# Performance work log

Measured on AMD Instinct MI355X. Metric: run time of the kernel, lower is better.

The kernel has to match this reference:

```python
import jax, jax.numpy as jnp
import numpy as np

B, H, S, DK = 2, 8, 4096, 64


def setup_inputs() -> dict:
    key = jax.random.key(0)
    kq, kk, kv = jax.random.split(key, 3)
    Q = jax.random.normal(kq, (B, H, S, DK), dtype=jnp.float32)
    K = jax.random.normal(kk, (B, H, S, DK), dtype=jnp.float32)
    V = jax.random.normal(kv, (B, H, S, DK), dtype=jnp.float32)
    attn_mask = jnp.zeros((1,), dtype=bool)  # accepted but unused by the module
    return {"Q": Q, "K": K, "V": V, "attn_mask": attn_mask}


def reference(Q, K, V, attn_mask):
    d_k = Q.shape[-1]
    scale = 1.0 / np.sqrt(d_k).astype(np.float32)
    # scores: [b, h, q, k] -- full O(n^2) matrix, as in the original
    scores = jnp.einsum('bhqd,bhkd->bhqk', Q, K) * scale
    attn = jax.nn.softmax(scores, axis=-1)
    context = jnp.einsum('bhqk,bhkd->bhqd', attn, V)
    return (context, attn)
```

## Files before the change

kernel.cpp:

```cpp
#include <hip/hip_runtime.h>
#include <hip/hip_bf16.h>


typedef __bf16 bf16x8 __attribute__((ext_vector_type(8)));
typedef __bf16 bf16x4 __attribute__((ext_vector_type(4)));
typedef float f32x4 __attribute__((ext_vector_type(4)));

#define BH 16
#define SEQ 4096
#define DKD 64

__global__ void cvt_bf16_kernel(const float* __restrict__ src,
                                __bf16* __restrict__ dst, int n4, float scale) {
    int i = blockIdx.x * blockDim.x + threadIdx.x;
    if (i < n4) {
        const float4 v = reinterpret_cast<const float4*>(src)[i];
        bf16x4 o;
        o[0] = (__bf16)(v.x * scale); o[1] = (__bf16)(v.y * scale);
        o[2] = (__bf16)(v.z * scale); o[3] = (__bf16)(v.w * scale);
        reinterpret_cast<bf16x4*>(dst)[i] = o;
    }
}

__global__ void transpose_v_kernel(const float* __restrict__ V,
                                   __bf16* __restrict__ Vt) {
    __shared__ __bf16 T[DKD][72];
    const int head = blockIdx.y;
    const int s0 = blockIdx.x * 64;
    const int t = threadIdx.x;
    const float* vp = V + ((size_t)head * SEQ + s0) * DKD;
#pragma unroll
    for (int i = 0; i < 16; ++i) {
        int j = i * 256 + t;
        T[j & 63][j >> 6] = (__bf16)vp[j];
    }
    __syncthreads();
    __bf16* op = Vt + (size_t)head * DKD * SEQ + s0;
#pragma unroll
    for (int i = 0; i < 16; ++i) {
        int j = i * 256 + t;
        op[(size_t)(j >> 6) * SEQ + (j & 63)] = T[j >> 6][j & 63];
    }
}

__global__ __launch_bounds__(128, 4) void attn_kernel(
    const __bf16* __restrict__ Qb, const __bf16* __restrict__ Kb,
    const __bf16* __restrict__ Vt, float* __restrict__ out_ctx,
    float* __restrict__ out_attn) {
    __shared__ __align__(16) float P32[2][16][68];

    const int tid = threadIdx.x;
    const int w = tid >> 6;
    const int lane = tid & 63;
    const int c16 = lane & 15;
    const int g = lane >> 4;
    const int head = blockIdx.y;
    const int qbase = blockIdx.x * 32 + w * 16;

    const __bf16* qp = Qb + ((size_t)head * SEQ + qbase + c16) * DKD + g * 8;
    const bf16x8 qf0 = *reinterpret_cast<const bf16x8*>(qp);
    const bf16x8 qf1 = *reinterpret_cast<const bf16x8*>(qp + 32);

    const __bf16* kbase = Kb + (size_t)head * SEQ * DKD;

    float lsum[4] = {0.f, 0.f, 0.f, 0.f};
    for (int kt = 0; kt < SEQ; kt += 64) {
        f32x4 acc[4];
#pragma unroll
        for (int ct = 0; ct < 4; ++ct) {
            acc[ct] = (f32x4){0.f, 0.f, 0.f, 0.f};
            const __bf16* kp = kbase + (size_t)(kt + ct * 16 + c16) * DKD + g * 8;
            bf16x8 kf0 = *reinterpret_cast<const bf16x8*>(kp);
            bf16x8 kf1 = *reinterpret_cast<const bf16x8*>(kp + 32);
            acc[ct] = __builtin_amdgcn_mfma_f32_16x16x32_bf16(qf0, kf0, acc[ct], 0, 0, 0);
            acc[ct] = __builtin_amdgcn_mfma_f32_16x16x32_bf16(qf1, kf1, acc[ct], 0, 0, 0);
        }
#pragma unroll
        for (int r = 0; r < 4; ++r) {
            lsum[r] += (__expf(acc[0][r]) + __expf(acc[1][r])) +
                       (__expf(acc[2][r]) + __expf(acc[3][r]));
        }
    }

    float inv_l[4];
#pragma unroll
    for (int r = 0; r < 4; ++r) {
        float t = lsum[r];
        t += __shfl_xor(t, 1);
        t += __shfl_xor(t, 2);
        t += __shfl_xor(t, 4);
        t += __shfl_xor(t, 8);
        inv_l[r] = 1.0f / t;
    }

    f32x4 o[4];
#pragma unroll
    for (int dt = 0; dt < 4; ++dt) o[dt] = (f32x4){0.f, 0.f, 0.f, 0.f};

    float* attn_p = out_attn + ((size_t)head * SEQ + qbase) * SEQ;
    const __bf16* vbase = Vt + (size_t)head * DKD * SEQ;

    for (int kt = 0; kt < SEQ; kt += 64) {
        f32x4 acc[4];
#pragma unroll
        for (int ct = 0; ct < 4; ++ct) {
            acc[ct] = (f32x4){0.f, 0.f, 0.f, 0.f};
            const __bf16* kp = kbase + (size_t)(kt + ct * 16 + c16) * DKD + g * 8;
            bf16x8 kf0 = *reinterpret_cast<const bf16x8*>(kp);
            bf16x8 kf1 = *reinterpret_cast<const bf16x8*>(kp + 32);
            acc[ct] = __builtin_amdgcn_mfma_f32_16x16x32_bf16(qf0, kf0, acc[ct], 0, 0, 0);
            acc[ct] = __builtin_amdgcn_mfma_f32_16x16x32_bf16(qf1, kf1, acc[ct], 0, 0, 0);
        }
#pragma unroll
        for (int ct = 0; ct < 4; ++ct) {
#pragma unroll
            for (int r = 0; r < 4; ++r) {
                P32[w][g * 4 + r][ct * 16 + c16] = __expf(acc[ct][r]) * inv_l[r];
            }
        }
        asm volatile("" ::: "memory");

#pragma unroll
        for (int r4 = 0; r4 < 4; ++r4) {
            const int row = r4 * 4 + g;
            f32x4 v = *reinterpret_cast<const f32x4*>(&P32[w][row][c16 * 4]);
            __builtin_nontemporal_store(
                v, reinterpret_cast<f32x4*>(attn_p + (size_t)row * SEQ + kt + c16 * 4));
        }

        f32x4 pr0 = *reinterpret_cast<const f32x4*>(&P32[w][c16][g * 8]);
        f32x4 pr1 = *reinterpret_cast<const f32x4*>(&P32[w][c16][g * 8 + 4]);
        f32x4 pr2 = *reinterpret_cast<const f32x4*>(&P32[w][c16][g * 8 + 32]);
        f32x4 pr3 = *reinterpret_cast<const f32x4*>(&P32[w][c16][g * 8 + 36]);
        bf16x8 pa0, pa1;
#pragma unroll
        for (int j = 0; j < 4; ++j) {
            pa0[j] = (__bf16)pr0[j];
            pa0[j + 4] = (__bf16)pr1[j];
            pa1[j] = (__bf16)pr2[j];
            pa1[j + 4] = (__bf16)pr3[j];
        }
#pragma unroll
        for (int dt = 0; dt < 4; ++dt) {
            const __bf16* vp2 = vbase + (size_t)(dt * 16 + c16) * SEQ + kt + g * 8;
            bf16x8 vf0 = *reinterpret_cast<const bf16x8*>(vp2);
            bf16x8 vf1 = *reinterpret_cast<const bf16x8*>(vp2 + 32);
            o[dt] = __builtin_amdgcn_mfma_f32_16x16x32_bf16(pa0, vf0, o[dt], 0, 0, 0);
            o[dt] = __builtin_amdgcn_mfma_f32_16x16x32_bf16(pa1, vf1, o[dt], 0, 0, 0);
        }
        asm volatile("" ::: "memory");
    }

    float* ctx_p = out_ctx + ((size_t)head * SEQ + qbase) * DKD;
#pragma unroll
    for (int dt = 0; dt < 4; ++dt)
#pragma unroll
        for (int r = 0; r < 4; ++r)
            ctx_p[(size_t)(g * 4 + r) * DKD + dt * 16 + c16] = o[dt][r];
}

extern "C" void kernel_launch(void* const* d_in, const int* in_sizes, int n_in,
                              void* d_out, int out_size, void* d_ws, size_t ws_size,
                              hipStream_t stream) {
    const float* Q = (const float*)d_in[0];
    const float* K = (const float*)d_in[1];
    const float* V = (const float*)d_in[2];
    float* out = (float*)d_out;

    const size_t nElem = (size_t)BH * SEQ * DKD;
    __bf16* Qb = (__bf16*)d_ws;
    __bf16* Kb = Qb + nElem;
    __bf16* Vt = Kb + nElem;

    float* out_ctx = out;
    float* out_attn = out + nElem;

    const int n4 = (int)(nElem / 4);
    cvt_bf16_kernel<<<dim3((n4 + 255) / 256), dim3(256), 0, stream>>>(Q, Qb, n4, 0.125f);
    cvt_bf16_kernel<<<dim3((n4 + 255) / 256), dim3(256), 0, stream>>>(K, Kb, n4, 1.0f);
    transpose_v_kernel<<<dim3(64, BH), dim3(256), 0, stream>>>(V, Vt);
    attn_kernel<<<dim3(SEQ / 32, BH), dim3(128), 0, stream>>>(Qb, Kb, Vt, out_ctx, out_attn);
}
```

Baseline: 726.1 us.

## Swap MFMA operand order, fold log2e into Q scale, software-pipeline S and PV

Swaps the MFMA operands so each lane holds a contiguous run of four scores for one query row. That lets the fp32 attention probabilities be stored straight from registers, drops the fp32 LDS staging, and cuts the row-sum reduction to two shuffles. The log2e factor is folded into the Q conversion scale so the kernel can use the hardware exp2 and rcp instructions. The bf16 P tile goes through double-buffered LDS, and computing the next S tile is interleaved with the PV MFMAs of the previous one to overlap the two. The occupancy hint in launch_bounds is removed, so register pressure may rise, and the fast exp2/rcp paths may cost some accuracy.

Result: no change. 734.8 us (+1.2%).

```diff
diff --git a/kernel.cpp b/kernel.cpp
--- a/kernel.cpp
+++ b/kernel.cpp
@@ -9,6 +9,7 @@
 #define BH 16
 #define SEQ 4096
 #define DKD 64
+#define PSTRIDE 72
 
 __global__ void cvt_bf16_kernel(const float* __restrict__ src,
                                 __bf16* __restrict__ dst, int n4, float scale) {
@@ -43,11 +44,11 @@
     }
 }
 
-__global__ __launch_bounds__(128, 4) void attn_kernel(
+__global__ __launch_bounds__(128) void attn_kernel(
     const __bf16* __restrict__ Qb, const __bf16* __restrict__ Kb,
     const __bf16* __restrict__ Vt, float* __restrict__ out_ctx,
     float* __restrict__ out_attn) {
-    __shared__ __align__(16) float P32[2][16][68];
+    __shared__ __align__(16) __bf16 Pl[2][2][16][PSTRIDE];
 
     const int tid = threadIdx.x;
     const int w = tid >> 6;
@@ -62,8 +63,10 @@
     const bf16x8 qf1 = *reinterpret_cast<const bf16x8*>(qp + 32);
 
     const __bf16* kbase = Kb + (size_t)head * SEQ * DKD;
+    const __bf16* vbase = Vt + (size_t)head * DKD * SEQ;
+    float* attn_p = out_attn + ((size_t)head * SEQ + qbase) * SEQ;
 
-    float lsum[4] = {0.f, 0.f, 0.f, 0.f};
+    float lsum = 0.f;
     for (int kt = 0; kt < SEQ; kt += 64) {
         f32x4 acc[4];
 #pragma unroll
@@ -72,35 +75,28 @@
             const __bf16* kp = kbase + (size_t)(kt + ct * 16 + c16) * DKD + g * 8;
             bf16x8 kf0 = *reinterpret_cast<const bf16x8*>(kp);
             bf16x8 kf1 = *reinterpret_cast<const bf16x8*>(kp + 32);
-            acc[ct] = __builtin_amdgcn_mfma_f32_16x16x32_bf16(qf0, kf0, acc[ct], 0, 0, 0);
-            acc[ct] = __builtin_amdgcn_mfma_f32_16x16x32_bf16(qf1, kf1, acc[ct], 0, 0, 0);
+            acc[ct] = __builtin_amdgcn_mfma_f32_16x16x32_bf16(kf0, qf0, acc[ct], 0, 0, 0);
+            acc[ct] = __builtin_amdgcn_mfma_f32_16x16x32_bf16(kf1, qf1, acc[ct], 0, 0, 0);
         }
 #pragma unroll
-        for (int r = 0; r < 4; ++r) {
-            lsum[r] += (__expf(acc[0][r]) + __expf(acc[1][r])) +
-                       (__expf(acc[2][r]) + __expf(acc[3][r]));
+        for (int ct = 0; ct < 4; ++ct) {
+            float e0 = __builtin_amdgcn_exp2f(acc[ct][0]);
+            float e1 = __builtin_amdgcn_exp2f(acc[ct][1]);
+            float e2 = __builtin_amdgcn_exp2f(acc[ct][2]);
+            float e3 = __builtin_amdgcn_exp2f(acc[ct][3]);
+            lsum += (e0 + e1) + (e2 + e3);
         }
     }
-
-    float inv_l[4];
-#pragma unroll
-    for (int r = 0; r < 4; ++r) {
-        float t = lsum[r];
-        t += __shfl_xor(t, 1);
-        t += __shfl_xor(t, 2);
-        t += __shfl_xor(t, 4);
-        t += __shfl_xor(t, 8);
-        inv_l[r] = 1.0f / t;
-    }
+    lsum += __shfl_xor(lsum, 16);
+    lsum += __shfl_xor(lsum, 32);
+    float inv_l = __builtin_amdgcn_rcpf(lsum);
 
     f32x4 o[4];
 #pragma unroll
     for (int dt = 0; dt < 4; ++dt) o[dt] = (f32x4){0.f, 0.f, 0.f, 0.f};
 
-    float* attn_p = out_attn + ((size_t)head * SEQ + qbase) * SEQ;
-    const __bf16* vbase = Vt + (size_t)head * DKD * SEQ;
-
-    for (int kt = 0; kt < SEQ; kt += 64) {
+    auto computeS = [&](int tile, __bf16(*Pbuf)[PSTRIDE]) {
+        const int kt = tile * 64;
         f32x4 acc[4];
 #pragma unroll
         for (int ct = 0; ct < 4; ++ct) {
@@ -108,55 +104,53 @@
             const __bf16* kp = kbase + (size_t)(kt + ct * 16 + c16) * DKD + g * 8;
             bf16x8 kf0 = *reinterpret_cast<const bf16x8*>(kp);
             bf16x8 kf1 = *reinterpret_cast<const bf16x8*>(kp + 32);
-            acc[ct] = __builtin_amdgcn_mfma_f32_16x16x32_bf16(qf0, kf0, acc[ct], 0, 0, 0);
-            acc[ct] = __builtin_amdgcn_mfma_f32_16x16x32_bf16(qf1, kf1, acc[ct], 0, 0, 0);
+            acc[ct] = __builtin_amdgcn_mfma_f32_16x16x32_bf16(kf0, qf0, acc[ct], 0, 0, 0);
+            acc[ct] = __builtin_amdgcn_mfma_f32_16x16x32_bf16(kf1, qf1, acc[ct], 0, 0, 0);
         }
 #pragma unroll
         for (int ct = 0; ct < 4; ++ct) {
+            f32x4 p;
 #pragma unroll
-            for (int r = 0; r < 4; ++r) {
-                P32[w][g * 4 + r][ct * 16 + c16] = __expf(acc[ct][r]) * inv_l[r];
-            }
+            for (int r = 0; r < 4; ++r)
+                p[r] = __builtin_amdgcn_exp2f(acc[ct][r]) * inv_l;
+            __builtin_nontemporal_store(
+                p, reinterpret_cast<f32x4*>(attn_p + (size_t)c16 * SEQ + kt + ct * 16 + g * 4));
+            bf16x4 pb;
+#pragma unroll
+            for (int r = 0; r < 4; ++r) pb[r] = (__bf16)p[r];
+            *reinterpret_cast<bf16x4*>(&Pbuf[c16][ct * 16 + g * 4]) = pb;
         }
-        asm volatile("" ::: "memory");
+    };
 
-#pragma unroll
-        for (int r4 = 0; r4 < 4; ++r4) {
-            const int row = r4 * 4 + g;
-            f32x4 v = *reinterpret_cast<const f32x4*>(&P32[w][row][c16 * 4]);
-            __builtin_nontemporal_store(
-                v, reinterpret_cast<f32x4*>(attn_p + (size_t)row * SEQ + kt + c16 * 4));
-        }
-
-        f32x4 pr0 = *reinterpret_cast<const f32x4*>(&P32[w][c16][g * 8]);
-        f32x4 pr1 = *reinterpret_cast<const f32x4*>(&P32[w][c16][g * 8 + 4]);
-        f32x4 pr2 = *reinterpret_cast<const f32x4*>(&P32[w][c16][g * 8 + 32]);
-        f32x4 pr3 = *reinterpret_cast<const f32x4*>(&P32[w][c16][g * 8 + 36]);
-        bf16x8 pa0, pa1;
-#pragma unroll
-        for (int j = 0; j < 4; ++j) {
-            pa0[j] = (__bf16)pr0[j];
-            pa0[j + 4] = (__bf16)pr1[j];
-            pa1[j] = (__bf16)pr2[j];
-            pa1[j + 4] = (__bf16)pr3[j];
-        }
+    auto pvTile = [&](int tile, const __bf16(*Pbuf)[PSTRIDE]) {
+        const int kt = tile * 64;
+        bf16x8 pb0 = *reinterpret_cast<const bf16x8*>(&Pbuf[c16][g * 8]);
+        bf16x8 pb1 = *reinterpret_cast<const bf16x8*>(&Pbuf[c16][g * 8 + 32]);
 #pragma unroll
         for (int dt = 0; dt < 4; ++dt) {
-            const __bf16* vp2 = vbase + (size_t)(dt * 16 + c16) * SEQ + kt + g * 8;
-            bf16x8 vf0 = *reinterpret_cast<const bf16x8*>(vp2);
-            bf16x8 vf1 = *reinterpret_cast<const bf16x8*>(vp2 + 32);
-            o[dt] = __builtin_amdgcn_mfma_f32_16x16x32_bf16(pa0, vf0, o[dt], 0, 0, 0);
-            o[dt] = __builtin_amdgcn_mfma_f32_16x16x32_bf16(pa1, vf1, o[dt], 0, 0, 0);
+            const __bf16* vp = vbase + (size_t)(dt * 16 + c16) * SEQ + kt + g * 8;
+            bf16x8 vf0 = *reinterpret_cast<const bf16x8*>(vp);
+            bf16x8 vf1 = *reinterpret_cast<const bf16x8*>(vp + 32);
+            o[dt] = __builtin_amdgcn_mfma_f32_16x16x32_bf16(vf0, pb0, o[dt], 0, 0, 0);
+            o[dt] = __builtin_amdgcn_mfma_f32_16x16x32_bf16(vf1, pb1, o[dt], 0, 0, 0);
         }
-        asm volatile("" ::: "memory");
+    };
+
+    computeS(0, Pl[0][w]);
+    for (int t = 1; t < 63; t += 2) {
+        computeS(t, Pl[1][w]);
+        pvTile(t - 1, Pl[0][w]);
+        computeS(t + 1, Pl[0][w]);
+        pvTile(t, Pl[1][w]);
     }
+    computeS(63, Pl[1][w]);
+    pvTile(62, Pl[0][w]);
+    pvTile(63, Pl[1][w]);
 
     float* ctx_p = out_ctx + ((size_t)head * SEQ + qbase) * DKD;
 #pragma unroll
     for (int dt = 0; dt < 4; ++dt)
-#pragma unroll
-        for (int r = 0; r < 4; ++r)
-            ctx_p[(size_t)(g * 4 + r) * DKD + dt * 16 + c16] = o[dt][r];
+        *reinterpret_cast<f32x4*>(ctx_p + (size_t)c16 * DKD + dt * 16 + g * 4) = o[dt];
 }
 
 extern "C" void kernel_launch(void* const* d_in, const int* in_sizes, int n_in,
@@ -176,7 +170,8 @@
     float* out_attn = out + nElem;
 
     const int n4 = (int)(nElem / 4);
-    cvt_bf16_kernel<<<dim3((n4 + 255) / 256), dim3(256), 0, stream>>>(Q, Qb, n4, 0.125f);
+    cvt_bf16_kernel<<<dim3((n4 + 255) / 256), dim3(256), 0, stream>>>(
+        Q, Qb, n4, 0.125f * 1.44269504088896f);
     cvt_bf16_kernel<<<dim3((n4 + 255) / 256), dim3(256), 0, stream>>>(K, Kb, n4, 1.0f);
     transpose_v_kernel<<<dim3(64, BH), dim3(256), 0, stream>>>(V, Vt);
     attn_kernel<<<dim3(SEQ / 32, BH), dim3(128), 0, stream>>>(Qb, Kb, Vt, out_ctx, out_attn);
```
